# Kernel optimization log

Hardware: AMD Instinct MI355X
Metric: run time of the kernel (lower is better)

Reference implementation:

```python
import jax, jax.numpy as jnp
import numpy as np

B, S, H, I, E, TOPK, KS = 4, 4096, 1024, 512, 16, 2, 3


def setup_inputs() -> dict:
    key = jax.random.key(0)
    ks = jax.random.split(key, 9)
    sc = 0.02
    return {
        "hidden_states": jax.random.normal(ks[0], (B, S, H), dtype=jnp.float32),
        "router_w": jax.random.normal(ks[1], (H, E), dtype=jnp.float32) * sc,
        "router_bias": jnp.zeros((E,), dtype=jnp.float32),
        "expert_gate_w": jax.random.normal(ks[2], (E - 1, H, I), dtype=jnp.float32) * sc,
        "expert_up_w": jax.random.normal(ks[3], (E - 1, H, I), dtype=jnp.float32) * sc,
        "expert_down_w": jax.random.normal(ks[4], (E - 1, I, H), dtype=jnp.float32) * sc,
        "conv_w": jax.random.normal(ks[5], (I, H, KS), dtype=jnp.float32) * sc,
        "shared_up_w": jax.random.normal(ks[6], (H, I), dtype=jnp.float32) * sc,
        "shared_down_w": jax.random.normal(ks[7], (I, H), dtype=jnp.float32) * sc,
    }


def reference(hidden_states, router_w, router_bias, expert_gate_w, expert_up_w,
              expert_down_w, conv_w, shared_up_w, shared_down_w):
    b, s, h = hidden_states.shape
    flat = hidden_states.reshape(b * s, h)  # (T, H)

    # ---- Router (mlp type, temperature=1, no noise at eval) ----
    logits = (flat @ router_w).astype(jnp.float32) + router_bias  # (T, E)
    probs = jax.nn.softmax(logits, axis=-1)
    top_w, top_i = jax.lax.top_k(probs, TOPK)  # (T, K)
    norm_w = top_w / (jnp.sum(top_w, axis=-1, keepdims=True) + 1e-6)
    norm_w = norm_w.astype(hidden_states.dtype)
    # Dense combine weights (T, E): scatter top-k weights into expert slots
    combine = jnp.sum(jax.nn.one_hot(top_i, E, dtype=norm_w.dtype) * norm_w[..., None], axis=1)

    # ---- Routed experts: E-1 SwiGLU MLPs + 1 Identity (index E-1) ----
    routed = combine[:, E - 1:E] * flat  # identity expert contribution
    for e in range(E - 1):
        y = (jax.nn.silu(flat @ expert_gate_w[e]) * (flat @ expert_up_w[e])) @ expert_down_w[e]
        routed = routed + combine[:, e:e + 1] * y
    routed = routed.reshape(b, s, h)

    # ---- Shared expert: causal conv1d gate * up, then down ----
    x_ncw = jnp.transpose(hidden_states, (0, 2, 1))  # (B, H, S)
    gate = jax.lax.conv_general_dilated(
        x_ncw, conv_w, window_strides=(1,), padding=[(KS - 1, 0)],
        dimension_numbers=("NCW", "OIW", "NCW"))  # (B, I, S)
    gate = jnp.transpose(gate, (0, 2, 1))  # (B, S, I)
    shared = (jax.nn.silu(gate) * (hidden_states @ shared_up_w)) @ shared_down_w

    return shared + routed
```

## Files before the change

### kernel.cpp

```cpp
#include <hip/hip_runtime.h>

typedef unsigned short u16;
typedef __attribute__((ext_vector_type(4))) float f32x4;
using bf16x8 = __attribute__((ext_vector_type(8))) short;
typedef __attribute__((ext_vector_type(8))) unsigned short u16x8;
typedef __attribute__((ext_vector_type(4))) unsigned short u16x4;

#define GAS __attribute__((address_space(1)))
#define LAS __attribute__((address_space(3)))

__device__ __forceinline__ float bf2f(u16 u) {
  unsigned v = ((unsigned)u) << 16;
  float f;
  __builtin_memcpy(&f, &v, 4);
  return f;
}
__device__ __forceinline__ u16 f2bf(float f) {
  unsigned u;
  __builtin_memcpy(&u, &f, 4);
  u += 0x7fffu + ((u >> 16) & 1u);
  return (u16)(u >> 16);
}
__device__ __forceinline__ void llds16(const void* g, void* l) {
  __builtin_amdgcn_global_load_lds((const GAS unsigned*)g, (LAS unsigned*)l, 16, 0, 0);
}

__global__ void cvtx_k(const float* __restrict__ x, u16* __restrict__ xb) {
  const long i = (long)blockIdx.x * 256 + threadIdx.x;
  f32x4 v = *(const f32x4*)(x + i * 4);
  u16x4 r;
#pragma unroll
  for (int j = 0; j < 4; ++j) r[j] = f2bf(v[j]);
  *(u16x4*)(xb + i * 4) = r;
}

__global__ __launch_bounds__(256) void router_k(const float* __restrict__ x,
    const float* __restrict__ rw, const float* __restrict__ rb,
    int* __restrict__ topk_idx, float* __restrict__ topk_w, int* __restrict__ ib) {
  __shared__ float xs[4][32 * 65];
  __shared__ float wsm[4][32 * 16];
  __shared__ float part[4][64 * 17];
  __shared__ int cnt[16];
  const int tid = threadIdx.x;
  const int wv = __builtin_amdgcn_readfirstlane(tid >> 6);
  const int lane = tid & 63;
  const int tok0 = blockIdx.x * 64;
  const int rr = lane >> 3;
  const int c4 = (lane & 7) * 4;

  float acc[16];
#pragma unroll
  for (int e = 0; e < 16; ++e) acc[e] = 0.f;

  for (int c = 0; c < 8; ++c) {
    const int hb = wv * 256 + c * 32;
    {
      f32x4 wa = *(const f32x4*)(rw + hb * 16 + lane * 4);
      f32x4 wb = *(const f32x4*)(rw + hb * 16 + 256 + lane * 4);
      *(f32x4*)&wsm[wv][lane * 4] = wa;
      *(f32x4*)&wsm[wv][256 + lane * 4] = wb;
    }
#pragma unroll
    for (int i = 0; i < 8; ++i) {
      const int row = i * 8 + rr;
      f32x4 v = *(const f32x4*)(x + (long)(tok0 + row) * 1024 + hb + c4);
#pragma unroll
      for (int j = 0; j < 4; ++j) xs[wv][(c4 + j) * 65 + row] = v[j];
    }
    __syncthreads();
#pragma unroll
    for (int h = 0; h < 32; ++h) {
      const float xv = xs[wv][h * 65 + lane];
      const float* wrow = &wsm[wv][h * 16];
#pragma unroll
      for (int q = 0; q < 4; ++q) {
        f32x4 w4 = *(const f32x4*)(wrow + q * 4);
#pragma unroll
        for (int e = 0; e < 4; ++e) acc[q * 4 + e] += xv * w4[e];
      }
    }
    __syncthreads();
  }
#pragma unroll
  for (int e = 0; e < 16; ++e) part[wv][lane * 17 + e] = acc[e];
  if (tid < 16) cnt[tid] = 0;
  __syncthreads();
  if (tid < 64) {
    float p[16];
#pragma unroll
    for (int e = 0; e < 16; ++e)
      p[e] = part[0][tid * 17 + e] + part[1][tid * 17 + e] +
             part[2][tid * 17 + e] + part[3][tid * 17 + e] + rb[e];
    float mx = p[0];
#pragma unroll
    for (int e = 1; e < 16; ++e) mx = fmaxf(mx, p[e]);
    float sum = 0.f;
#pragma unroll
    for (int e = 0; e < 16; ++e) { p[e] = __expf(p[e] - mx); sum += p[e]; }
    int i0 = 0; float p0 = p[0];
    for (int e = 1; e < 16; ++e) if (p[e] > p0) { p0 = p[e]; i0 = e; }
    int i1 = -1; float p1 = -1.f;
    for (int e = 0; e < 16; ++e) if (e != i0 && p[e] > p1) { p1 = p[e]; i1 = e; }
    const float inv = 1.f / sum;
    p0 *= inv; p1 *= inv;
    const float d = p0 + p1 + 1e-6f;
    const int t = tok0 + tid;
    topk_idx[t * 2] = i0; topk_idx[t * 2 + 1] = i1;
    topk_w[t * 2] = p0 / d;
    topk_w[t * 2 + 1] = p1 / d;
    if (i0 < 15) atomicAdd(&cnt[i0], 1);
    if (i1 < 15) atomicAdd(&cnt[i1], 1);
  }
  __syncthreads();
  if (tid < 15 && cnt[tid] > 0) atomicAdd(&ib[tid], cnt[tid]);
}

__global__ void zero_k(int* __restrict__ ib) {
  if (threadIdx.x < 16) ib[threadIdx.x] = 0;
}

__global__ void scan_k(int* __restrict__ ib) {
  if (threadIdx.x != 0 || blockIdx.x != 0) return;
  int off = 0;
  for (int ee = 0; ee < 15; ++ee) { ib[16 + ee] = off; ib[32 + ee] = off; off += ib[ee]; }
  ib[16 + 15] = off;
  int nm = 0;
  for (int ee = 0; ee < 15; ++ee) {
    const int st = ib[16 + ee], en = ib[16 + ee + 1];
    for (int r = st; r < en; r += 128) {
      ib[64 + nm * 4] = ee; ib[64 + nm * 4 + 1] = r; ib[64 + nm * 4 + 2] = en; ++nm;
    }
  }
  ib[48] = nm;
}

__global__ __launch_bounds__(256) void scatter_k(const int* __restrict__ topk_idx,
                          const float* __restrict__ topk_w,
                          int* __restrict__ ib, int* __restrict__ tok_ids,
                          float* __restrict__ tok_w, int* __restrict__ slot_map) {
  __shared__ int cnt[16], base[16];
  const int tid = threadIdx.x;
  const int j = blockIdx.x * 256 + tid;
  if (tid < 16) cnt[tid] = 0;
  __syncthreads();
  const int e = topk_idx[j];
  int lo = 0;
  if (e < 15) lo = atomicAdd(&cnt[e], 1);
  __syncthreads();
  if (tid < 15 && cnt[tid] > 0) base[tid] = atomicAdd(&ib[32 + tid], cnt[tid]);
  __syncthreads();
  if (e < 15) {
    const int pos = base[e] + lo;
    tok_ids[pos] = j >> 1;
    tok_w[pos] = topk_w[j];
    slot_map[j] = pos;
  } else {
    slot_map[j] = -1;
  }
}

__global__ void transpose_k(const float* __restrict__ src, u16* __restrict__ dst, int R, int C) {
  __shared__ float tile[32][33];
  src += (long)blockIdx.z * R * C;
  dst += (long)blockIdx.z * R * C;
  const int c0 = blockIdx.x * 32, r0 = blockIdx.y * 32;
  const int tx = threadIdx.x & 31, ty = threadIdx.x >> 5;
#pragma unroll
  for (int i = ty; i < 32; i += 8) tile[i][tx] = src[(long)(r0 + i) * C + c0 + tx];
  __syncthreads();
#pragma unroll
  for (int i = ty; i < 32; i += 8) dst[(long)(c0 + i) * R + r0 + tx] = f2bf(tile[tx][i]);
}

__global__ void convt_k(const float* __restrict__ cw, u16* __restrict__ dst) {
  const int idx = blockIdx.x * 256 + threadIdx.x;
  if (idx >= 3 * 512 * 1024) return;
  const int k = idx >> 19;
  const int rem = idx & 524287;
  const int i = rem >> 10, h = rem & 1023;
  dst[idx] = f2bf(cw[i * 3072 + h * 3 + k]);
}

template<int V>
__global__ __launch_bounds__(256, 2)
void gemm_k(const u16* __restrict__ Abase, const u16* __restrict__ Bt0,
            const u16* __restrict__ Bt1, void* __restrict__ OUTv,
            const int* __restrict__ tbl, const int* __restrict__ nmt,
            const int* __restrict__ tok_ids, const float* __restrict__ tok_w,
            int K, int ldA, int ldOut) {
  __shared__ u16 lds[24576];
  u16* OUT = (u16*)OUTv;
  float* OUTF = (float*)OUTv;
  const int tid = threadIdx.x;
  const int wave = tid >> 6, lane = tid & 63;
  const int quad = lane >> 4, l16 = lane & 15;
  const int rA = tid >> 2;
  const int sub8 = (tid & 3) * 8;
  const int sub8s = ((tid & 3) ^ ((tid >> 3) & 3)) * 8;

  constexpr int NYC = (V == 2 || V == 3) ? 4 : 8;
  const int lin = (blockIdx.x & 7) * (gridDim.x >> 3) + (blockIdx.x >> 3);
  const int bx = lin / NYC, by = lin - bx * NYC;

  int e = 0, row0, row_end;
  if constexpr (V <= 1) {
    if (bx >= *nmt) return;
    e = tbl[bx * 4]; row0 = tbl[bx * 4 + 1]; row_end = tbl[bx * 4 + 2];
  } else {
    row0 = bx * 128; row_end = row0 + 128;
  }
  const int n0 = by * ((V == 0) ? 64 : 128);

  f32x4 acc[2][8];
#pragma unroll
  for (int i = 0; i < 2; ++i)
#pragma unroll
    for (int j = 0; j < 8; ++j) acc[i][j] = (f32x4){0.f, 0.f, 0.f, 0.f};

  const int swz8 = (((l16 >> 1) & 3) ^ quad) * 8;
  const int aoff0 = (wave * 32 + l16) * 32 + swz8;
  const int aoff1 = aoff0 + 512;
  const int kIters = K / 32;

  if constexpr (V != 3) {
    const u16 *pA0, *pA1, *pB0, *pB1;
    if constexpr (V == 0) {
      const int t0i = tok_ids[min(row0 + rA, row_end - 1)];
      const int t1i = tok_ids[min(row0 + rA + 64, row_end - 1)];
      pA0 = Abase + (long)t0i * 1024 + sub8s;
      pA1 = Abase + (long)t1i * 1024 + sub8s;
      pB0 = Bt0 + ((long)e * 512 + n0 + rA) * 1024 + sub8s;
      pB1 = Bt1 + ((long)e * 512 + n0 + rA) * 1024 + sub8s;
    } else if constexpr (V == 1) {
      pA0 = Abase + (long)min(row0 + rA, row_end - 1) * 512 + sub8s;
      pA1 = Abase + (long)min(row0 + rA + 64, row_end - 1) * 512 + sub8s;
      pB0 = Bt0 + ((long)e * 1024 + n0 + rA) * 512 + sub8s;
      pB1 = Bt0 + ((long)e * 1024 + n0 + rA + 64) * 512 + sub8s;
    } else {
      pA0 = Abase + (long)(row0 + rA) * ldA + sub8s;
      pA1 = Abase + (long)(row0 + rA + 64) * ldA + sub8s;
      pB0 = Bt0 + (long)(n0 + rA) * K + sub8s;
      pB1 = Bt0 + (long)(n0 + rA + 64) * K + sub8s;
    }
    auto STAGE = [&](int buf) {
      llds16(pA0, &lds[buf + wave * 512]); pA0 += 32;
      llds16(pA1, &lds[buf + 2048 + wave * 512]); pA1 += 32;
      llds16(pB0, &lds[buf + 4096 + wave * 512]); pB0 += 32;
      llds16(pB1, &lds[buf + 6144 + wave * 512]); pB1 += 32;
    };
    STAGE(0);
    STAGE(8192);
    int cur = 0, stg = 16384;
    for (int kb = 0; kb < kIters; ++kb) {
      if (kb + 1 < kIters) {
        asm volatile("s_waitcnt vmcnt(4)" ::: "memory");
      } else {
        asm volatile("s_waitcnt vmcnt(0)" ::: "memory");
      }
      __builtin_amdgcn_s_barrier();
      if (kb + 2 < kIters) {
        STAGE(stg);
        stg = (stg == 16384) ? 0 : stg + 8192;
      }
      bf16x8 a0 = *(const bf16x8*)&lds[cur + aoff0];
      bf16x8 a1 = *(const bf16x8*)&lds[cur + aoff1];
      __builtin_amdgcn_s_setprio(1);
#pragma unroll
      for (int nt = 0; nt < 8; ++nt) {
        bf16x8 b = *(const bf16x8*)&lds[cur + 4096 + (nt * 16 + l16) * 32 + swz8];
        acc[0][nt] = __builtin_amdgcn_mfma_f32_16x16x32_bf16(a0, b, acc[0][nt], 0, 0, 0);
        acc[1][nt] = __builtin_amdgcn_mfma_f32_16x16x32_bf16(a1, b, acc[1][nt], 0, 0, 0);
      }
      __builtin_amdgcn_s_setprio(0);
      cur = (cur == 16384) ? 0 : cur + 8192;
    }
    __builtin_amdgcn_s_barrier();
  } else {
    int cur = 0;
    u16x8 va0n, va1n;
    for (int ph = 0; ph < 3; ++ph) {
      const u16 *pA0, *pA1, *pB0, *pB1;
      const int bb = row0 >> 12, s0 = row0 & 4095;
      const int si0 = s0 + ph - 2 + rA;
      const bool zero0 = si0 < 0;
      pA0 = Abase + ((long)bb * 4096 + (si0 < 0 ? 0 : si0)) * 1024 + sub8s;
      pA1 = Abase + ((long)bb * 4096 + (si0 + 64)) * 1024 + sub8s;
      pB0 = Bt0 + (long)ph * 512 * 1024 + (long)(n0 + rA) * 1024 + sub8s;
      pB1 = Bt0 + (long)ph * 512 * 1024 + (long)(n0 + rA + 64) * 1024 + sub8s;

      va0n = *(const u16x8*)pA0; pA0 += 32;
      va1n = *(const u16x8*)pA1; pA1 += 32;
      if (zero0) va0n = (u16x8){0, 0, 0, 0, 0, 0, 0, 0};
      *(u16x8*)&lds[cur + rA * 32 + sub8] = va0n;
      *(u16x8*)&lds[cur + (rA + 64) * 32 + sub8] = va1n;
      llds16(pB0, &lds[cur + 4096 + wave * 512]); pB0 += 32;
      llds16(pB1, &lds[cur + 6144 + wave * 512]); pB1 += 32;
      __syncthreads();

      for (int kb = 0; kb < kIters; ++kb) {
        const int nxt = cur ^ 8192;
        const bool pre = (kb + 1 < kIters);
        if (pre) {
          llds16(pB0, &lds[nxt + 4096 + wave * 512]); pB0 += 32;
          llds16(pB1, &lds[nxt + 6144 + wave * 512]); pB1 += 32;
          va0n = *(const u16x8*)pA0; pA0 += 32;
          va1n = *(const u16x8*)pA1; pA1 += 32;
          if (zero0) va0n = (u16x8){0, 0, 0, 0, 0, 0, 0, 0};
        }
        bf16x8 a0 = *(const bf16x8*)&lds[cur + aoff0];
        bf16x8 a1 = *(const bf16x8*)&lds[cur + aoff1];
#pragma unroll
        for (int nt = 0; nt < 8; ++nt) {
          bf16x8 b = *(const bf16x8*)&lds[cur + 4096 + (nt * 16 + l16) * 32 + swz8];
          acc[0][nt] = __builtin_amdgcn_mfma_f32_16x16x32_bf16(a0, b, acc[0][nt], 0, 0, 0);
          acc[1][nt] = __builtin_amdgcn_mfma_f32_16x16x32_bf16(a1, b, acc[1][nt], 0, 0, 0);
        }
        if (pre) {
          *(u16x8*)&lds[nxt + rA * 32 + sub8] = va0n;
          *(u16x8*)&lds[nxt + (rA + 64) * 32 + sub8] = va1n;
        }
        __syncthreads();
        cur = nxt;
      }
    }
  }

  const int rbase = wave * 32;
  if constexpr (V == 0) {
#pragma unroll
    for (int mt = 0; mt < 2; ++mt)
#pragma unroll
      for (int r = 0; r < 4; ++r) {
        const int row = rbase + mt * 16 + quad * 4 + r;
#pragma unroll
        for (int nt = 0; nt < 4; ++nt) {
          float g = acc[mt][nt][r], u = acc[mt][nt + 4][r];
          float sg = g / (1.f + __expf(-g));
          lds[row * 64 + nt * 16 + l16] = f2bf(sg * u);
        }
      }
    __syncthreads();
#pragma unroll
    for (int i = 0; i < 4; ++i) {
      const int c = i * 256 + tid;
      const int row = c >> 3, s8 = (c & 7) * 8;
      const int slot = row0 + row;
      if (slot < row_end)
        *(u16x8*)(OUT + (long)slot * ldOut + n0 + s8) = *(const u16x8*)&lds[row * 64 + s8];
    }
  } else if constexpr (V == 1) {
#pragma unroll
    for (int mt = 0; mt < 2; ++mt)
#pragma unroll
      for (int r = 0; r < 4; ++r) {
        const int row = rbase + mt * 16 + quad * 4 + r;
        const float wgt = tok_w[min(row0 + row, row_end - 1)];
#pragma unroll
        for (int nt = 0; nt < 8; ++nt)
          lds[row * 128 + nt * 16 + l16] = f2bf(acc[mt][nt][r] * wgt);
      }
    __syncthreads();
#pragma unroll
    for (int i = 0; i < 8; ++i) {
      const int c = i * 256 + tid;
      const int row = c >> 4, s8 = (c & 15) * 8;
      const int slot = row0 + row;
      if (slot < row_end)
        *(u16x8*)(OUT + (long)slot * ldOut + n0 + s8) = *(const u16x8*)&lds[row * 128 + s8];
    }
  } else if constexpr (V == 2) {
#pragma unroll
    for (int mt = 0; mt < 2; ++mt)
#pragma unroll
      for (int r = 0; r < 4; ++r) {
        const int row = rbase + mt * 16 + quad * 4 + r;
#pragma unroll
        for (int nt = 0; nt < 8; ++nt)
          lds[row * 128 + nt * 16 + l16] = f2bf(acc[mt][nt][r]);
      }
    __syncthreads();
#pragma unroll
    for (int i = 0; i < 8; ++i) {
      const int c = i * 256 + tid;
      const int row = c >> 4, s8 = (c & 15) * 8;
      *(u16x8*)(OUT + (long)(row0 + row) * ldOut + n0 + s8) = *(const u16x8*)&lds[row * 128 + s8];
    }
  } else if constexpr (V == 3) {
#pragma unroll
    for (int mt = 0; mt < 2; ++mt)
#pragma unroll
      for (int r = 0; r < 4; ++r) {
        const int row = rbase + mt * 16 + quad * 4 + r;
#pragma unroll
        for (int nt = 0; nt < 8; ++nt) {
          float g = acc[mt][nt][r];
          lds[row * 128 + nt * 16 + l16] = f2bf(g / (1.f + __expf(-g)));
        }
      }
    __syncthreads();
#pragma unroll
    for (int i = 0; i < 8; ++i) {
      const int c = i * 256 + tid;
      const int row = c >> 4, s8 = (c & 15) * 8;
      const long o = (long)(row0 + row) * ldOut + n0 + s8;
      u16x8 sg8 = *(const u16x8*)&lds[row * 128 + s8];
      u16x8 up8 = *(const u16x8*)(OUT + o);
      u16x8 res;
#pragma unroll
      for (int j = 0; j < 8; ++j) res[j] = f2bf(bf2f(sg8[j]) * bf2f(up8[j]));
      *(u16x8*)(OUT + o) = res;
    }
  } else {
#pragma unroll
    for (int mt = 0; mt < 2; ++mt)
#pragma unroll
      for (int r = 0; r < 4; ++r) {
        const int row = row0 + rbase + mt * 16 + quad * 4 + r;
#pragma unroll
        for (int nt = 0; nt < 8; ++nt)
          OUTF[(long)row * ldOut + n0 + nt * 16 + l16] = acc[mt][nt][r];
      }
  }
}

__global__ void final_k(const float* __restrict__ x, const u16* __restrict__ Y,
                        const int* __restrict__ slot_map, const float* __restrict__ topk_w,
                        float* __restrict__ out) {
  const long idx = (long)blockIdx.x * 256 + threadIdx.x;
  const int t = (int)(idx >> 8), cc = ((int)idx & 255) * 4;
  const long ob = (long)t * 1024 + cc;
  f32x4 o = *(const f32x4*)(out + ob);
#pragma unroll
  for (int k2 = 0; k2 < 2; ++k2) {
    const int sm = slot_map[t * 2 + k2];
    if (sm >= 0) {
      u16x4 y = *(const u16x4*)(Y + (long)sm * 1024 + cc);
#pragma unroll
      for (int j = 0; j < 4; ++j) o[j] += bf2f(y[j]);
    } else {
      const float w = topk_w[t * 2 + k2];
      f32x4 xv = *(const f32x4*)(x + ob);
#pragma unroll
      for (int j = 0; j < 4; ++j) o[j] += w * xv[j];
    }
  }
  *(f32x4*)(out + ob) = o;
}

extern "C" void kernel_launch(void* const* d_in, const int* in_sizes, int n_in,
                              void* d_out, int out_size, void* d_ws, size_t ws_size,
                              hipStream_t stream) {
  (void)in_sizes; (void)n_in; (void)out_size; (void)ws_size;
  const float* x   = (const float*)d_in[0];
  const float* rw  = (const float*)d_in[1];
  const float* rb  = (const float*)d_in[2];
  const float* gw  = (const float*)d_in[3];
  const float* uw  = (const float*)d_in[4];
  const float* dw  = (const float*)d_in[5];
  const float* cw  = (const float*)d_in[6];
  const float* suw = (const float*)d_in[7];
  const float* sdw = (const float*)d_in[8];
  float* out = (float*)d_out;

  char* base = (char*)d_ws;
  size_t off = 0;
  auto alloc = [&](size_t b) { void* p = base + off; off = (off + b + 255) & ~(size_t)255; return p; };
  u16* xb     = (u16*)alloc(16777216ull * 2);
  u16* gate_t = (u16*)alloc(15ull * 512 * 1024 * 2);
  u16* up_t   = (u16*)alloc(15ull * 512 * 1024 * 2);
  u16* down_t = (u16*)alloc(15ull * 1024 * 512 * 2);
  u16* conv_t = (u16*)alloc(3ull * 512 * 1024 * 2);
  u16* sup_t  = (u16*)alloc(512ull * 1024 * 2);
  u16* sdn_t  = (u16*)alloc(512ull * 1024 * 2);
  u16* inter  = (u16*)alloc(32768ull * 512 * 2);
  u16* Y      = (u16*)alloc(32768ull * 1024 * 2);
  u16* UP     = (u16*)alloc(16384ull * 512 * 2);
  int*   topi    = (int*)alloc(32768 * 4);
  float* topw    = (float*)alloc(32768 * 4);
  int*   smap    = (int*)alloc(32768 * 4);
  int*   tok_ids = (int*)alloc(32768 * 4);
  float* tokw    = (float*)alloc(32768 * 4);
  int*   ib      = (int*)alloc(8192);

  zero_k<<<1, 64, 0, stream>>>(ib);
  cvtx_k<<<16384, 256, 0, stream>>>(x, xb);
  transpose_k<<<dim3(16, 32, 15), 256, 0, stream>>>(gw, gate_t, 1024, 512);
  transpose_k<<<dim3(16, 32, 15), 256, 0, stream>>>(uw, up_t, 1024, 512);
  transpose_k<<<dim3(32, 16, 15), 256, 0, stream>>>(dw, down_t, 512, 1024);
  transpose_k<<<dim3(16, 32, 1), 256, 0, stream>>>(suw, sup_t, 1024, 512);
  transpose_k<<<dim3(32, 16, 1), 256, 0, stream>>>(sdw, sdn_t, 512, 1024);
  convt_k<<<6144, 256, 0, stream>>>(cw, conv_t);
  router_k<<<256, 256, 0, stream>>>(x, rw, rb, topi, topw, ib);
  scan_k<<<1, 64, 0, stream>>>(ib);
  scatter_k<<<128, 256, 0, stream>>>(topi, topw, ib, tok_ids, tokw, smap);
  gemm_k<0><<<2176, 256, 0, stream>>>(xb, gate_t, up_t, inter, ib + 64, ib + 48,
                                      tok_ids, tokw, 1024, 1024, 512);
  gemm_k<1><<<2176, 256, 0, stream>>>(inter, down_t, nullptr, Y, ib + 64, ib + 48,
                                      nullptr, tokw, 512, 512, 1024);
  gemm_k<2><<<512, 256, 0, stream>>>(xb, sup_t, nullptr, UP, nullptr, nullptr,
                                     nullptr, nullptr, 1024, 1024, 512);
  gemm_k<3><<<512, 256, 0, stream>>>(xb, conv_t, nullptr, UP, nullptr, nullptr,
                                     nullptr, nullptr, 1024, 1024, 512);
  gemm_k<4><<<1024, 256, 0, stream>>>(UP, sdn_t, nullptr, out, nullptr, nullptr,
                                      nullptr, nullptr, 512, 512, 1024);
  final_k<<<16384, 256, 0, stream>>>(x, Y, smap, topw, out);
}
```

Measured before the change: 565.2 us.

## Fuse bf16 cast into router, shared up into conv GEMM, combine into down GEMM

Three fusions remove separate passes. The bf16 cast of x moves into the router kernel, which already reads x. The shared-expert up projection is computed as a second accumulator inside the conv-gate GEMM, so the SiLU(gate)*up product is formed in registers and the read-modify-write of UP goes away. The final combine kernel is folded into the shared down-projection epilogue, which gathers Y rows or the identity-expert x directly. In exchange, the conv GEMM holds twice the accumulator registers, and the down-GEMM epilogue does scalar gathers that are not coalesced.

```diff
diff --git a/kernel.cpp b/kernel.cpp
--- a/kernel.cpp
+++ b/kernel.cpp
@@ -25,18 +25,10 @@
   __builtin_amdgcn_global_load_lds((const GAS unsigned*)g, (LAS unsigned*)l, 16, 0, 0);
 }
 
-__global__ void cvtx_k(const float* __restrict__ x, u16* __restrict__ xb) {
-  const long i = (long)blockIdx.x * 256 + threadIdx.x;
-  f32x4 v = *(const f32x4*)(x + i * 4);
-  u16x4 r;
-#pragma unroll
-  for (int j = 0; j < 4; ++j) r[j] = f2bf(v[j]);
-  *(u16x4*)(xb + i * 4) = r;
-}
-
 __global__ __launch_bounds__(256) void router_k(const float* __restrict__ x,
     const float* __restrict__ rw, const float* __restrict__ rb,
-    int* __restrict__ topk_idx, float* __restrict__ topk_w, int* __restrict__ ib) {
+    int* __restrict__ topk_idx, float* __restrict__ topk_w, int* __restrict__ ib,
+    u16* __restrict__ xb) {
   __shared__ float xs[4][32 * 65];
   __shared__ float wsm[4][32 * 16];
   __shared__ float part[4][64 * 17];
@@ -63,9 +55,15 @@
 #pragma unroll
     for (int i = 0; i < 8; ++i) {
       const int row = i * 8 + rr;
-      f32x4 v = *(const f32x4*)(x + (long)(tok0 + row) * 1024 + hb + c4);
-#pragma unroll
-      for (int j = 0; j < 4; ++j) xs[wv][(c4 + j) * 65 + row] = v[j];
+      const long gb = (long)(tok0 + row) * 1024 + hb + c4;
+      f32x4 v = *(const f32x4*)(x + gb);
+      u16x4 b4;
+#pragma unroll
+      for (int j = 0; j < 4; ++j) {
+        xs[wv][(c4 + j) * 65 + row] = v[j];
+        b4[j] = f2bf(v[j]);
+      }
+      *(u16x4*)(xb + gb) = b4;
     }
     __syncthreads();
 #pragma unroll
@@ -198,7 +196,7 @@
   const int sub8 = (tid & 3) * 8;
   const int sub8s = ((tid & 3) ^ ((tid >> 3) & 3)) * 8;
 
-  constexpr int NYC = (V == 2 || V == 3) ? 4 : 8;
+  constexpr int NYC = (V == 3) ? 4 : 8;
   const int lin = (blockIdx.x & 7) * (gridDim.x >> 3) + (blockIdx.x >> 3);
   const int bx = lin / NYC, by = lin - bx * NYC;
 
@@ -212,10 +210,14 @@
   const int n0 = by * ((V == 0) ? 64 : 128);
 
   f32x4 acc[2][8];
+  f32x4 acc2[2][8];
 #pragma unroll
   for (int i = 0; i < 2; ++i)
 #pragma unroll
-    for (int j = 0; j < 8; ++j) acc[i][j] = (f32x4){0.f, 0.f, 0.f, 0.f};
+    for (int j = 0; j < 8; ++j) {
+      acc[i][j] = (f32x4){0.f, 0.f, 0.f, 0.f};
+      if constexpr (V == 3) acc2[i][j] = (f32x4){0.f, 0.f, 0.f, 0.f};
+    }
 
   const int swz8 = (((l16 >> 1) & 3) ^ quad) * 8;
   const int aoff0 = (wave * 32 + l16) * 32 + swz8;
@@ -278,15 +280,15 @@
   } else {
     int cur = 0;
     u16x8 va0n, va1n;
+    const int bb = row0 >> 12, s0 = row0 & 4095;
     for (int ph = 0; ph < 3; ++ph) {
       const u16 *pA0, *pA1, *pB0, *pB1;
-      const int bb = row0 >> 12, s0 = row0 & 4095;
       const int si0 = s0 + ph - 2 + rA;
       const bool zero0 = si0 < 0;
       pA0 = Abase + ((long)bb * 4096 + (si0 < 0 ? 0 : si0)) * 1024 + sub8s;
       pA1 = Abase + ((long)bb * 4096 + (si0 + 64)) * 1024 + sub8s;
-      pB0 = Bt0 + (long)ph * 512 * 1024 + (long)(n0 + rA) * 1024 + sub8s;
-      pB1 = Bt0 + (long)ph * 512 * 1024 + (long)(n0 + rA + 64) * 1024 + sub8s;
+      pB0 = Bt0 + (long)ph * 524288 + (long)(n0 + rA) * 1024 + sub8s;
+      pB1 = Bt0 + (long)ph * 524288 + (long)(n0 + rA + 64) * 1024 + sub8s;
 
       va0n = *(const u16x8*)pA0; pA0 += 32;
       va1n = *(const u16x8*)pA1; pA1 += 32;
@@ -323,6 +325,45 @@
         cur = nxt;
       }
     }
+    {
+      const u16* pA0 = Abase + ((long)bb * 4096 + s0 + rA) * 1024 + sub8s;
+      const u16* pA1 = Abase + ((long)bb * 4096 + s0 + rA + 64) * 1024 + sub8s;
+      const u16* pB0 = Bt1 + (long)(n0 + rA) * 1024 + sub8s;
+      const u16* pB1 = Bt1 + (long)(n0 + rA + 64) * 1024 + sub8s;
+
+      va0n = *(const u16x8*)pA0; pA0 += 32;
+      va1n = *(const u16x8*)pA1; pA1 += 32;
+      *(u16x8*)&lds[cur + rA * 32 + sub8] = va0n;
+      *(u16x8*)&lds[cur + (rA + 64) * 32 + sub8] = va1n;
+      llds16(pB0, &lds[cur + 4096 + wave * 512]); pB0 += 32;
+      llds16(pB1, &lds[cur + 6144 + wave * 512]); pB1 += 32;
+      __syncthreads();
+
+      for (int kb = 0; kb < kIters; ++kb) {
+        const int nxt = cur ^ 8192;
+        const bool pre = (kb + 1 < kIters);
+        if (pre) {
+          llds16(pB0, &lds[nxt + 4096 + wave * 512]); pB0 += 32;
+          llds16(pB1, &lds[nxt + 6144 + wave * 512]); pB1 += 32;
+          va0n = *(const u16x8*)pA0; pA0 += 32;
+          va1n = *(const u16x8*)pA1; pA1 += 32;
+        }
+        bf16x8 a0 = *(const bf16x8*)&lds[cur + aoff0];
+        bf16x8 a1 = *(const bf16x8*)&lds[cur + aoff1];
+#pragma unroll
+        for (int nt = 0; nt < 8; ++nt) {
+          bf16x8 b = *(const bf16x8*)&lds[cur + 4096 + (nt * 16 + l16) * 32 + swz8];
+          acc2[0][nt] = __builtin_amdgcn_mfma_f32_16x16x32_bf16(a0, b, acc2[0][nt], 0, 0, 0);
+          acc2[1][nt] = __builtin_amdgcn_mfma_f32_16x16x32_bf16(a1, b, acc2[1][nt], 0, 0, 0);
+        }
+        if (pre) {
+          *(u16x8*)&lds[nxt + rA * 32 + sub8] = va0n;
+          *(u16x8*)&lds[nxt + (rA + 64) * 32 + sub8] = va1n;
+        }
+        __syncthreads();
+        cur = nxt;
+      }
+    }
   }
 
   const int rbase = wave * 32;
@@ -368,15 +409,17 @@
       if (slot < row_end)
         *(u16x8*)(OUT + (long)slot * ldOut + n0 + s8) = *(const u16x8*)&lds[row * 128 + s8];
     }
-  } else if constexpr (V == 2) {
+  } else if constexpr (V == 3) {
 #pragma unroll
     for (int mt = 0; mt < 2; ++mt)
 #pragma unroll
       for (int r = 0; r < 4; ++r) {
         const int row = rbase + mt * 16 + quad * 4 + r;
 #pragma unroll
-        for (int nt = 0; nt < 8; ++nt)
-          lds[row * 128 + nt * 16 + l16] = f2bf(acc[mt][nt][r]);
+        for (int nt = 0; nt < 8; ++nt) {
+          float g = acc[mt][nt][r], u = acc2[mt][nt][r];
+          lds[row * 128 + nt * 16 + l16] = f2bf(g / (1.f + __expf(-g)) * u);
+        }
       }
     __syncthreads();
 #pragma unroll
@@ -385,66 +428,28 @@
       const int row = c >> 4, s8 = (c & 15) * 8;
       *(u16x8*)(OUT + (long)(row0 + row) * ldOut + n0 + s8) = *(const u16x8*)&lds[row * 128 + s8];
     }
-  } else if constexpr (V == 3) {
-#pragma unroll
-    for (int mt = 0; mt < 2; ++mt)
-#pragma unroll
-      for (int r = 0; r < 4; ++r) {
-        const int row = rbase + mt * 16 + quad * 4 + r;
-#pragma unroll
-        for (int nt = 0; nt < 8; ++nt) {
-          float g = acc[mt][nt][r];
-          lds[row * 128 + nt * 16 + l16] = f2bf(g / (1.f + __expf(-g)));
-        }
-      }
-    __syncthreads();
-#pragma unroll
-    for (int i = 0; i < 8; ++i) {
-      const int c = i * 256 + tid;
-      const int row = c >> 4, s8 = (c & 15) * 8;
-      const long o = (long)(row0 + row) * ldOut + n0 + s8;
-      u16x8 sg8 = *(const u16x8*)&lds[row * 128 + s8];
-      u16x8 up8 = *(const u16x8*)(OUT + o);
-      u16x8 res;
-#pragma unroll
-      for (int j = 0; j < 8; ++j) res[j] = f2bf(bf2f(sg8[j]) * bf2f(up8[j]));
-      *(u16x8*)(OUT + o) = res;
-    }
   } else {
+    const u16* Yb = Bt1;
+    const float* xf = (const float*)tok_ids;
 #pragma unroll
     for (int mt = 0; mt < 2; ++mt)
 #pragma unroll
       for (int r = 0; r < 4; ++r) {
         const int row = row0 + rbase + mt * 16 + quad * 4 + r;
-#pragma unroll
-        for (int nt = 0; nt < 8; ++nt)
-          OUTF[(long)row * ldOut + n0 + nt * 16 + l16] = acc[mt][nt][r];
-      }
-  }
-}
-
-__global__ void final_k(const float* __restrict__ x, const u16* __restrict__ Y,
-                        const int* __restrict__ slot_map, const float* __restrict__ topk_w,
-                        float* __restrict__ out) {
-  const long idx = (long)blockIdx.x * 256 + threadIdx.x;
-  const int t = (int)(idx >> 8), cc = ((int)idx & 255) * 4;
-  const long ob = (long)t * 1024 + cc;
-  f32x4 o = *(const f32x4*)(out + ob);
-#pragma unroll
-  for (int k2 = 0; k2 < 2; ++k2) {
-    const int sm = slot_map[t * 2 + k2];
-    if (sm >= 0) {
-      u16x4 y = *(const u16x4*)(Y + (long)sm * 1024 + cc);
-#pragma unroll
-      for (int j = 0; j < 4; ++j) o[j] += bf2f(y[j]);
-    } else {
-      const float w = topk_w[t * 2 + k2];
-      f32x4 xv = *(const f32x4*)(x + ob);
-#pragma unroll
-      for (int j = 0; j < 4; ++j) o[j] += w * xv[j];
-    }
-  }
-  *(f32x4*)(out + ob) = o;
+        const int sm0 = tbl[row * 2], sm1 = tbl[row * 2 + 1];
+        const float w0 = tok_w[row * 2], w1 = tok_w[row * 2 + 1];
+#pragma unroll
+        for (int nt = 0; nt < 8; ++nt) {
+          const int col = n0 + nt * 16 + l16;
+          float o = acc[mt][nt][r];
+          if (sm0 >= 0) o += bf2f(Yb[(long)sm0 * 1024 + col]);
+          else          o += w0 * xf[(long)row * 1024 + col];
+          if (sm1 >= 0) o += bf2f(Yb[(long)sm1 * 1024 + col]);
+          else          o += w1 * xf[(long)row * 1024 + col];
+          OUTF[(long)row * ldOut + col] = o;
+        }
+      }
+  }
 }
 
 extern "C" void kernel_launch(void* const* d_in, const int* in_sizes, int n_in,
@@ -483,25 +488,21 @@
   int*   ib      = (int*)alloc(8192);
 
   zero_k<<<1, 64, 0, stream>>>(ib);
-  cvtx_k<<<16384, 256, 0, stream>>>(x, xb);
   transpose_k<<<dim3(16, 32, 15), 256, 0, stream>>>(gw, gate_t, 1024, 512);
   transpose_k<<<dim3(16, 32, 15), 256, 0, stream>>>(uw, up_t, 1024, 512);
   transpose_k<<<dim3(32, 16, 15), 256, 0, stream>>>(dw, down_t, 512, 1024);
   transpose_k<<<dim3(16, 32, 1), 256, 0, stream>>>(suw, sup_t, 1024, 512);
   transpose_k<<<dim3(32, 16, 1), 256, 0, stream>>>(sdw, sdn_t, 512, 1024);
   convt_k<<<6144, 256, 0, stream>>>(cw, conv_t);
-  router_k<<<256, 256, 0, stream>>>(x, rw, rb, topi, topw, ib);
+  router_k<<<256, 256, 0, stream>>>(x, rw, rb, topi, topw, ib, xb);
   scan_k<<<1, 64, 0, stream>>>(ib);
   scatter_k<<<128, 256, 0, stream>>>(topi, topw, ib, tok_ids, tokw, smap);
   gemm_k<0><<<2176, 256, 0, stream>>>(xb, gate_t, up_t, inter, ib + 64, ib + 48,
                                       tok_ids, tokw, 1024, 1024, 512);
   gemm_k<1><<<2176, 256, 0, stream>>>(inter, down_t, nullptr, Y, ib + 64, ib + 48,
                                       nullptr, tokw, 512, 512, 1024);
-  gemm_k<2><<<512, 256, 0, stream>>>(xb, sup_t, nullptr, UP, nullptr, nullptr,
+  gemm_k<3><<<512, 256, 0, stream>>>(xb, conv_t, sup_t, UP, nullptr, nullptr,
                                      nullptr, nullptr, 1024, 1024, 512);
-  gemm_k<3><<<512, 256, 0, stream>>>(xb, conv_t, nullptr, UP, nullptr, nullptr,
-                                     nullptr, nullptr, 1024, 1024, 512);
-  gemm_k<4><<<1024, 256, 0, stream>>>(UP, sdn_t, nullptr, out, nullptr, nullptr,
-                                      nullptr, nullptr, 512, 512, 1024);
-  final_k<<<16384, 256, 0, stream>>>(x, Y, smap, topw, out);
-}
+  gemm_k<4><<<1024, 256, 0, stream>>>(UP, sdn_t, Y, out, smap, nullptr,
+                                      (const int*)x, topw, 512, 512, 1024);
+}
```

Measured after the change: 603.5 us. 1.07x slower.
